# Optimization experiments

Measured on AMD Instinct MI355X. Metric: run time of the kernel, lower is better.

Reference implementation:

```python
import jax, jax.numpy as jnp
import numpy as np

LN_EPS = 1e-5  # torch LayerNorm default
MODES = 4


def setup_inputs() -> dict:
    key = jax.random.key(0)
    ks = jax.random.split(key, 5)
    B, S, H = 4, 4096, 1024
    nh, dk = 16, H // 16
    scale = 1.0 / (H * H)
    # frequency mode selection: random shuffle of range(S//2), take 4, sorted (seeded for determinism)
    rng = np.random.default_rng(0)
    index = jnp.asarray(np.sort(rng.permutation(S // 2)[:MODES]).astype(np.int32))
    return {
        "x": jax.random.normal(ks[0], (B, S, H), dtype=jnp.float32),
        "Wq": jax.random.normal(ks[1], (H, H), dtype=jnp.float32) * np.sqrt(2.0 / (H + dk)),
        "bq": jnp.zeros((H,), dtype=jnp.float32),
        "wr": scale * jax.random.uniform(ks[2], (nh, dk, dk, MODES), dtype=jnp.float32),
        "wi": scale * jax.random.uniform(ks[3], (nh, dk, dk, MODES), dtype=jnp.float32),
        "gamma": jnp.ones((H,), dtype=jnp.float32),
        "beta": jnp.zeros((H,), dtype=jnp.float32),
        "index": index,
    }


def reference(x, Wq, bq, wr, wi, gamma, beta, index):
    B, S, H = x.shape
    nh, dk = wr.shape[0], wr.shape[1]
    # q projection and head split: (B,S,H) -> (B,S,nh,dk) -> (B,nh,dk,S)
    q = (x @ Wq.T + bq).reshape(B, S, nh, dk).transpose(0, 2, 3, 1)
    x_ft = jnp.fft.rfft(q, axis=-1)                 # (B,nh,dk,S//2+1) complex
    xm = x_ft[..., index]                           # gather selected modes: (B,nh,dk,M)
    w = wr + 1j * wi                                # (nh,dk,dk,M) complex
    ym = jnp.einsum('bhim,hiom->bhom', xm, w)       # per-mode complex matmul
    # faithful: results written at slots 0..M-1 of out_ft (loop writes out_ft[...,wi])
    out_ft = jnp.zeros((B, nh, dk, S // 2 + 1), dtype=ym.dtype).at[..., :ym.shape[-1]].set(ym)
    x_if = jnp.fft.irfft(out_ft, n=S, axis=-1)      # (B,nh,dk,S) real
    # faithful permute(0,3,2,1).view: flattens as dk-major over heads
    out = x_if.transpose(0, 3, 2, 1).reshape(B, S, H)
    # dropout is identity in eval mode
    y = out + x
    mu = jnp.mean(y, axis=-1, keepdims=True)
    var = jnp.var(y, axis=-1, keepdims=True)
    return (y - mu) * jax.lax.rsqrt(var + LN_EPS) * gamma + beta
```

## Files before the change

### kernel.cpp

```cpp
#include <hip/hip_runtime.h>
#include <math.h>

#define BB 4
#define SS 4096
#define HH 1024
#define NH 16
#define DK 64
#define NMODES 4
#define NSB 128
#define SCHUNK (SS/NSB)
#define PPLANE ((size_t)BB * NSB * HH)
#define TWO_PI 6.28318530717958647692f

__global__ __launch_bounds__(256) void kA_dft(const float* __restrict__ x,
                                              const int* __restrict__ index,
                                              float* __restrict__ P) {
    __shared__ float tab[SCHUNK * 8];
    int t  = threadIdx.x;
    int sb = blockIdx.x & (NSB - 1);
    int b  = blockIdx.x >> 7;

    if (t < SCHUNK * NMODES) {
        int sl = t >> 2, m = t & 3;
        int k  = index[m];
        int sv = sb * SCHUNK + sl;
        int r  = (k * sv) & (SS - 1);
        float ang = (float)r * (TWO_PI / (float)SS);
        float sn, cs;
        sincosf(ang, &sn, &cs);
        tab[sl * 8 + m * 2]     = cs;
        tab[sl * 8 + m * 2 + 1] = sn;
    }
    __syncthreads();

    int c0 = t * 4;
    float acc[4][8];
    #pragma unroll
    for (int e = 0; e < 4; ++e)
        #pragma unroll
        for (int q = 0; q < 8; ++q) acc[e][q] = 0.f;

    const float* xp = x + ((size_t)(b * SS + sb * SCHUNK)) * HH + c0;
    #pragma unroll 8
    for (int r = 0; r < SCHUNK; ++r) {
        float4 xv = *(const float4*)(xp + (size_t)r * HH);
        float4 t0 = *(const float4*)&tab[r * 8];
        float4 t1 = *(const float4*)&tab[r * 8 + 4];
        float xe;
        #pragma unroll
        for (int e = 0; e < 4; ++e) {
            xe = (e == 0) ? xv.x : (e == 1) ? xv.y : (e == 2) ? xv.z : xv.w;
            acc[e][0] += xe * t0.x;  acc[e][1] -= xe * t0.y;
            acc[e][2] += xe * t0.z;  acc[e][3] -= xe * t0.w;
            acc[e][4] += xe * t1.x;  acc[e][5] -= xe * t1.y;
            acc[e][6] += xe * t1.z;  acc[e][7] -= xe * t1.w;
        }
    }
    size_t base = (size_t)(b * NSB + sb) * HH + c0;
    #pragma unroll
    for (int q = 0; q < 8; ++q) {
        *(float4*)&P[q * PPLANE + base] =
            make_float4(acc[0][q], acc[1][q], acc[2][q], acc[3][q]);
    }
}

__global__ __launch_bounds__(256) void kA2_reduce(const float* __restrict__ P,
                                                  float* __restrict__ G) {
    int i = blockIdx.x * 256 + threadIdx.x;
    int g = i >> 2;
    int quarter = i & 3;
    int j = g & (HH - 1);
    int q = (g >> 10) & 7;
    int b = g >> 13;
    const float* pp = P + q * PPLANE + (size_t)b * NSB * HH
                    + (size_t)(quarter * (NSB / 4)) * HH + j;
    float s = 0.f;
    #pragma unroll 16
    for (int sb = 0; sb < NSB / 4; ++sb)
        s += pp[(size_t)sb * HH];
    s += __shfl_xor(s, 1);
    s += __shfl_xor(s, 2);
    if (quarter == 0) G[g] = s;
}

__global__ __launch_bounds__(256) void kB_proj(const float* __restrict__ Wq,
                                               const float* __restrict__ bq,
                                               const int* __restrict__ index,
                                               const float* __restrict__ G,
                                               float* __restrict__ XM) {
    __shared__ float Gs[8 * HH];
    int t  = threadIdx.x;
    int cb = blockIdx.x & 63;
    int b  = blockIdx.x >> 6;
    {
        const float4* gsrc = (const float4*)(G + (size_t)b * 8 * HH);
        float4* gdst = (float4*)Gs;
        for (int u = t; u < 2 * HH; u += 256) gdst[u] = gsrc[u];
    }
    __syncthreads();

    int cl = t >> 4, jq = t & 15;
    int c = cb * 16 + cl;
    float acc[8] = {0.f,0.f,0.f,0.f,0.f,0.f,0.f,0.f};
    for (int j0 = jq * 4; j0 < HH; j0 += 64) {
        float4 wv = *(const float4*)&Wq[(size_t)c * HH + j0];
        #pragma unroll
        for (int q = 0; q < 8; ++q) {
            float4 gv = *(const float4*)&Gs[q * HH + j0];
            acc[q] += wv.x * gv.x + wv.y * gv.y + wv.z * gv.z + wv.w * gv.w;
        }
    }
    #pragma unroll
    for (int q = 0; q < 8; ++q) {
        acc[q] += __shfl_xor(acc[q], 1);
        acc[q] += __shfl_xor(acc[q], 2);
        acc[q] += __shfl_xor(acc[q], 4);
        acc[q] += __shfl_xor(acc[q], 8);
    }
    if (jq == 0) {
        float bias = bq[c];
        #pragma unroll
        for (int m = 0; m < NMODES; ++m)
            if (index[m] == 0) acc[2 * m] += bias * (float)SS;
        float* o = XM + ((size_t)(b * HH + c)) * 8;
        *(float4*)o       = make_float4(acc[0], acc[1], acc[2], acc[3]);
        *(float4*)(o + 4) = make_float4(acc[4], acc[5], acc[6], acc[7]);
    }
}

#define KC_IQ 8
#define KC_II (DK / KC_IQ)
__global__ __launch_bounds__(512) void kC_modes(const float* __restrict__ wr,
                                                const float* __restrict__ wi,
                                                const float* __restrict__ XM,
                                                float* __restrict__ CF) {
    __shared__ float xs[DK * 8];
    __shared__ float red[KC_IQ][DK][9];
    int t = threadIdx.x;
    int o = t & 63, iq = t >> 6;
    int h = blockIdx.x & 15;
    int b = blockIdx.x >> 4;
    for (int u = t; u < DK * 8; u += 512)
        xs[u] = XM[((size_t)(b * HH + h * DK)) * 8 + u];
    __syncthreads();

    float re[4] = {0.f,0.f,0.f,0.f}, im[4] = {0.f,0.f,0.f,0.f};
    #pragma unroll
    for (int ii = 0; ii < KC_II; ++ii) {
        int i = iq * KC_II + ii;
        float4 wrv = *(const float4*)&wr[(((size_t)(h * DK + i)) * DK + o) * 4];
        float4 wiv = *(const float4*)&wi[(((size_t)(h * DK + i)) * DK + o) * 4];
        float xr, xi;
        xr = xs[i * 8 + 0]; xi = xs[i * 8 + 1];
        re[0] += xr * wrv.x - xi * wiv.x;  im[0] += xr * wiv.x + xi * wrv.x;
        xr = xs[i * 8 + 2]; xi = xs[i * 8 + 3];
        re[1] += xr * wrv.y - xi * wiv.y;  im[1] += xr * wiv.y + xi * wrv.y;
        xr = xs[i * 8 + 4]; xi = xs[i * 8 + 5];
        re[2] += xr * wrv.z - xi * wiv.z;  im[2] += xr * wiv.z + xi * wrv.z;
        xr = xs[i * 8 + 6]; xi = xs[i * 8 + 7];
        re[3] += xr * wrv.w - xi * wiv.w;  im[3] += xr * wiv.w + xi * wrv.w;
    }
    #pragma unroll
    for (int m = 0; m < 4; ++m) {
        red[iq][o][2 * m]     = re[m];
        red[iq][o][2 * m + 1] = im[m];
    }
    __syncthreads();
    if (iq == 0) {
        float rr[8];
        #pragma unroll
        for (int q = 0; q < 8; ++q) {
            float s = 0.f;
            #pragma unroll
            for (int g = 0; g < KC_IQ; ++g) s += red[g][o][q];
            rr[q] = s;
        }
        int co = o * NH + h;
        const float inv = 1.0f / (float)SS;
        float* cp = CF + ((size_t)(b * HH + co)) * 8;
        cp[0] =  rr[0] * inv;
        cp[1] =  2.0f * rr[2] * inv;
        cp[2] = -2.0f * rr[3] * inv;
        cp[3] =  2.0f * rr[4] * inv;
        cp[4] = -2.0f * rr[5] * inv;
        cp[5] =  2.0f * rr[6] * inv;
        cp[6] = -2.0f * rr[7] * inv;
        cp[7] =  0.0f;
    }
}

#define KD_ROWS 8
__global__ __launch_bounds__(256) void kD_out(const float* __restrict__ x,
                                              const float* __restrict__ CF,
                                              const float* __restrict__ gamma,
                                              const float* __restrict__ beta,
                                              float* __restrict__ out) {
    __shared__ float trig[KD_ROWS][2];
    __shared__ float red[4][KD_ROWS][2];
    int t  = threadIdx.x;
    int b  = blockIdx.x >> 9;
    int s0 = (blockIdx.x & 511) * KD_ROWS;
    int c0 = t * 4;

    if (t < KD_ROWS) {
        float ang = (float)(s0 + t) * (TWO_PI / (float)SS);
        float sn, cs;
        sincosf(ang, &sn, &cs);
        trig[t][0] = cs;
        trig[t][1] = sn;
    }

    const float* cp = CF + (size_t)b * HH * 8 + (size_t)c0 * 8;
    float4 cfa[8];
    #pragma unroll
    for (int e = 0; e < 4; ++e) {
        cfa[2 * e]     = *(const float4*)(cp + e * 8);
        cfa[2 * e + 1] = *(const float4*)(cp + e * 8 + 4);
    }
    float4 g4 = *(const float4*)&gamma[c0];
    float4 b4 = *(const float4*)&beta[c0];
    int w = t >> 6, lane = t & 63;
    __syncthreads();

    float4 yv[KD_ROWS];
    #pragma unroll
    for (int r = 0; r < KD_ROWS; ++r) {
        int s = s0 + r;
        yv[r] = *(const float4*)&x[((size_t)(b * SS + s)) * HH + c0];
    }
    float sm[KD_ROWS], sq[KD_ROWS];
    #pragma unroll
    for (int r = 0; r < KD_ROWS; ++r) {
        float c1 = trig[r][0], s1 = trig[r][1];
        float c2 = c1 * c1 - s1 * s1, s2 = 2.f * s1 * c1;
        float c3 = c2 * c1 - s2 * s1, s3 = s2 * c1 + c2 * s1;
        float ye[4];
        #pragma unroll
        for (int e = 0; e < 4; ++e) {
            float xe = (e == 0) ? yv[r].x : (e == 1) ? yv[r].y
                     : (e == 2) ? yv[r].z : yv[r].w;
            float4 A = cfa[2 * e], Bv = cfa[2 * e + 1];
            ye[e] = xe + A.x + A.y * c1 + A.z * s1 + A.w * c2
                       + Bv.x * s2 + Bv.y * c3 + Bv.z * s3;
        }
        yv[r] = make_float4(ye[0], ye[1], ye[2], ye[3]);
        sm[r] = ye[0] + ye[1] + ye[2] + ye[3];
        sq[r] = ye[0]*ye[0] + ye[1]*ye[1] + ye[2]*ye[2] + ye[3]*ye[3];
    }
    #pragma unroll
    for (int off = 1; off < 64; off <<= 1) {
        #pragma unroll
        for (int r = 0; r < KD_ROWS; ++r) {
            sm[r] += __shfl_xor(sm[r], off);
            sq[r] += __shfl_xor(sq[r], off);
        }
    }
    if (lane == 0) {
        #pragma unroll
        for (int r = 0; r < KD_ROWS; ++r) {
            red[w][r][0] = sm[r];
            red[w][r][1] = sq[r];
        }
    }
    __syncthreads();
    #pragma unroll
    for (int r = 0; r < KD_ROWS; ++r) {
        int s = s0 + r;
        float tot  = red[0][r][0] + red[1][r][0] + red[2][r][0] + red[3][r][0];
        float totq = red[0][r][1] + red[1][r][1] + red[2][r][1] + red[3][r][1];
        float mean = tot * (1.0f / (float)HH);
        float var  = totq * (1.0f / (float)HH) - mean * mean;
        float rs = rsqrtf(var + 1e-5f);
        float4 o4;
        o4.x = (yv[r].x - mean) * rs * g4.x + b4.x;
        o4.y = (yv[r].y - mean) * rs * g4.y + b4.y;
        o4.z = (yv[r].z - mean) * rs * g4.z + b4.z;
        o4.w = (yv[r].w - mean) * rs * g4.w + b4.w;
        *(float4*)&out[((size_t)(b * SS + s)) * HH + c0] = o4;
    }
}

extern "C" void kernel_launch(void* const* d_in, const int* in_sizes, int n_in,
                              void* d_out, int out_size, void* d_ws, size_t ws_size,
                              hipStream_t stream) {
    const float* x     = (const float*)d_in[0];
    const float* Wq    = (const float*)d_in[1];
    const float* bq    = (const float*)d_in[2];
    const float* wr    = (const float*)d_in[3];
    const float* wi    = (const float*)d_in[4];
    const float* gamma = (const float*)d_in[5];
    const float* beta  = (const float*)d_in[6];
    const int*   index = (const int*)d_in[7];
    float* out = (float*)d_out;
    float* ws  = (float*)d_ws;

    const size_t nP     = PPLANE * 8;
    const size_t nSmall = (size_t)BB * HH * 8;

    float *P, *G, *XM, *CF;
    if (ws_size >= (nP + 3 * nSmall) * sizeof(float)) {
        P  = ws;
        G  = P + nP;
        XM = G + nSmall;
        CF = XM + nSmall;
    } else {
        P  = out;
        G  = ws;
        XM = G + nSmall;
        CF = XM + nSmall;
    }

    hipLaunchKernelGGL(kA_dft,     dim3(BB * NSB), dim3(256), 0, stream, x, index, P);
    hipLaunchKernelGGL(kA2_reduce, dim3(BB * HH * 8 * 4 / 256), dim3(256), 0, stream, P, G);
    hipLaunchKernelGGL(kB_proj,    dim3(BB * 64), dim3(256), 0, stream, Wq, bq, index, G, XM);
    hipLaunchKernelGGL(kC_modes,   dim3(BB * NH), dim3(512), 0, stream, wr, wi, XM, CF);
    hipLaunchKernelGGL(kD_out,     dim3(BB * (SS / KD_ROWS)), dim3(256), 0, stream, x, CF, gamma, beta, out);
}
```

Measured before the change: 58.63 us.

## Fuse DFT partial reduction in-block, merge projection and mode kernels, shuffle trig

```diff
diff --git a/kernel.cpp b/kernel.cpp
--- a/kernel.cpp
+++ b/kernel.cpp
@@ -7,23 +7,24 @@
 #define NH 16
 #define DK 64
 #define NMODES 4
-#define NSB 128
-#define SCHUNK (SS/NSB)
-#define PPLANE ((size_t)BB * NSB * HH)
 #define TWO_PI 6.28318530717958647692f
 
-__global__ __launch_bounds__(256) void kA_dft(const float* __restrict__ x,
+__global__ __launch_bounds__(512) void kA_dft(const float* __restrict__ x,
                                               const int* __restrict__ index,
-                                              float* __restrict__ P) {
-    __shared__ float tab[SCHUNK * 8];
-    int t  = threadIdx.x;
-    int sb = blockIdx.x & (NSB - 1);
-    int b  = blockIdx.x >> 7;
-
-    if (t < SCHUNK * NMODES) {
-        int sl = t >> 2, m = t & 3;
-        int k  = index[m];
-        int sv = sb * SCHUNK + sl;
+                                              float* __restrict__ Gp) {
+    __shared__ float tab[1024 * 8];
+    __shared__ float red[8][16][33];
+    int t   = threadIdx.x;
+    int bid = blockIdx.x;
+    int cb  = bid & 15;
+    int sq  = (bid >> 4) & 3;
+    int b   = bid >> 6;
+
+    int k0 = index[0], k1 = index[1], k2 = index[2], k3 = index[3];
+    for (int u = t; u < 4096; u += 512) {
+        int sl = u >> 2, m = u & 3;
+        int k  = (m == 0) ? k0 : (m == 1) ? k1 : (m == 2) ? k2 : k3;
+        int sv = sq * 1024 + sl;
         int r  = (k * sv) & (SS - 1);
         float ang = (float)r * (TWO_PI / (float)SS);
         float sn, cs;
@@ -33,19 +34,21 @@
     }
     __syncthreads();
 
-    int c0 = t * 4;
+    int c4 = t & 15, srow = t >> 4;
+    int c0 = cb * 64 + c4 * 4;
     float acc[4][8];
     #pragma unroll
     for (int e = 0; e < 4; ++e)
         #pragma unroll
         for (int q = 0; q < 8; ++q) acc[e][q] = 0.f;
 
-    const float* xp = x + ((size_t)(b * SS + sb * SCHUNK)) * HH + c0;
+    const float* xp = x + ((size_t)(b * SS + sq * 1024 + srow)) * HH + c0;
     #pragma unroll 8
-    for (int r = 0; r < SCHUNK; ++r) {
-        float4 xv = *(const float4*)(xp + (size_t)r * HH);
-        float4 t0 = *(const float4*)&tab[r * 8];
-        float4 t1 = *(const float4*)&tab[r * 8 + 4];
+    for (int pass = 0; pass < 32; ++pass) {
+        float4 xv = *(const float4*)(xp + (size_t)pass * 32 * HH);
+        int sl = pass * 32 + srow;
+        float4 t0 = *(const float4*)&tab[sl * 8];
+        float4 t1 = *(const float4*)&tab[sl * 8 + 4];
         float xe;
         #pragma unroll
         for (int e = 0; e < 4; ++e) {
@@ -56,136 +59,136 @@
             acc[e][6] += xe * t1.z;  acc[e][7] -= xe * t1.w;
         }
     }
-    size_t base = (size_t)(b * NSB + sb) * HH + c0;
-    #pragma unroll
-    for (int q = 0; q < 8; ++q) {
-        *(float4*)&P[q * PPLANE + base] =
-            make_float4(acc[0][q], acc[1][q], acc[2][q], acc[3][q]);
+    #pragma unroll
+    for (int e = 0; e < 4; ++e)
+        #pragma unroll
+        for (int q = 0; q < 8; ++q) {
+            acc[e][q] += __shfl_xor(acc[e][q], 16);
+            acc[e][q] += __shfl_xor(acc[e][q], 32);
+        }
+    int w = t >> 6, lane = t & 63;
+    if (lane < 16) {
+        #pragma unroll
+        for (int e = 0; e < 4; ++e)
+            #pragma unroll
+            for (int q = 0; q < 8; ++q)
+                red[w][lane][e * 8 + q] = acc[e][q];
+    }
+    __syncthreads();
+    {
+        int q = t >> 6, oc = t & 63;
+        float s = 0.f;
+        #pragma unroll
+        for (int w2 = 0; w2 < 8; ++w2)
+            s += red[w2][oc >> 2][(oc & 3) * 8 + q];
+        Gp[((size_t)((b * 4 + sq) * 8 + q)) * HH + cb * 64 + oc] = s;
     }
 }
 
-__global__ __launch_bounds__(256) void kA2_reduce(const float* __restrict__ P,
-                                                  float* __restrict__ G) {
-    int i = blockIdx.x * 256 + threadIdx.x;
-    int g = i >> 2;
-    int quarter = i & 3;
-    int j = g & (HH - 1);
-    int q = (g >> 10) & 7;
-    int b = g >> 13;
-    const float* pp = P + q * PPLANE + (size_t)b * NSB * HH
-                    + (size_t)(quarter * (NSB / 4)) * HH + j;
-    float s = 0.f;
-    #pragma unroll 16
-    for (int sb = 0; sb < NSB / 4; ++sb)
-        s += pp[(size_t)sb * HH];
-    s += __shfl_xor(s, 1);
-    s += __shfl_xor(s, 2);
-    if (quarter == 0) G[g] = s;
-}
-
-__global__ __launch_bounds__(256) void kB_proj(const float* __restrict__ Wq,
-                                               const float* __restrict__ bq,
-                                               const int* __restrict__ index,
-                                               const float* __restrict__ G,
-                                               float* __restrict__ XM) {
+__global__ __launch_bounds__(512) void kBC(const float* __restrict__ Gp,
+                                           const float* __restrict__ Wq,
+                                           const float* __restrict__ bq,
+                                           const int* __restrict__ index,
+                                           const float* __restrict__ wr,
+                                           const float* __restrict__ wi,
+                                           float* __restrict__ CF) {
     __shared__ float Gs[8 * HH];
-    int t  = threadIdx.x;
-    int cb = blockIdx.x & 63;
-    int b  = blockIdx.x >> 6;
-    {
-        const float4* gsrc = (const float4*)(G + (size_t)b * 8 * HH);
-        float4* gdst = (float4*)Gs;
-        for (int u = t; u < 2 * HH; u += 256) gdst[u] = gsrc[u];
-    }
-    __syncthreads();
-
-    int cl = t >> 4, jq = t & 15;
-    int c = cb * 16 + cl;
-    float acc[8] = {0.f,0.f,0.f,0.f,0.f,0.f,0.f,0.f};
-    for (int j0 = jq * 4; j0 < HH; j0 += 64) {
-        float4 wv = *(const float4*)&Wq[(size_t)c * HH + j0];
-        #pragma unroll
-        for (int q = 0; q < 8; ++q) {
-            float4 gv = *(const float4*)&Gs[q * HH + j0];
-            acc[q] += wv.x * gv.x + wv.y * gv.y + wv.z * gv.z + wv.w * gv.w;
-        }
-    }
-    #pragma unroll
-    for (int q = 0; q < 8; ++q) {
-        acc[q] += __shfl_xor(acc[q], 1);
-        acc[q] += __shfl_xor(acc[q], 2);
-        acc[q] += __shfl_xor(acc[q], 4);
-        acc[q] += __shfl_xor(acc[q], 8);
-    }
-    if (jq == 0) {
-        float bias = bq[c];
-        #pragma unroll
-        for (int m = 0; m < NMODES; ++m)
-            if (index[m] == 0) acc[2 * m] += bias * (float)SS;
-        float* o = XM + ((size_t)(b * HH + c)) * 8;
-        *(float4*)o       = make_float4(acc[0], acc[1], acc[2], acc[3]);
-        *(float4*)(o + 4) = make_float4(acc[4], acc[5], acc[6], acc[7]);
-    }
-}
-
-#define KC_IQ 8
-#define KC_II (DK / KC_IQ)
-__global__ __launch_bounds__(512) void kC_modes(const float* __restrict__ wr,
-                                                const float* __restrict__ wi,
-                                                const float* __restrict__ XM,
-                                                float* __restrict__ CF) {
     __shared__ float xs[DK * 8];
-    __shared__ float red[KC_IQ][DK][9];
+    __shared__ float red[8][DK][9];
     int t = threadIdx.x;
-    int o = t & 63, iq = t >> 6;
     int h = blockIdx.x & 15;
     int b = blockIdx.x >> 4;
-    for (int u = t; u < DK * 8; u += 512)
-        xs[u] = XM[((size_t)(b * HH + h * DK)) * 8 + u];
-    __syncthreads();
-
-    float re[4] = {0.f,0.f,0.f,0.f}, im[4] = {0.f,0.f,0.f,0.f};
-    #pragma unroll
-    for (int ii = 0; ii < KC_II; ++ii) {
-        int i = iq * KC_II + ii;
-        float4 wrv = *(const float4*)&wr[(((size_t)(h * DK + i)) * DK + o) * 4];
-        float4 wiv = *(const float4*)&wi[(((size_t)(h * DK + i)) * DK + o) * 4];
-        float xr, xi;
-        xr = xs[i * 8 + 0]; xi = xs[i * 8 + 1];
-        re[0] += xr * wrv.x - xi * wiv.x;  im[0] += xr * wiv.x + xi * wrv.x;
-        xr = xs[i * 8 + 2]; xi = xs[i * 8 + 3];
-        re[1] += xr * wrv.y - xi * wiv.y;  im[1] += xr * wiv.y + xi * wrv.y;
-        xr = xs[i * 8 + 4]; xi = xs[i * 8 + 5];
-        re[2] += xr * wrv.z - xi * wiv.z;  im[2] += xr * wiv.z + xi * wrv.z;
-        xr = xs[i * 8 + 6]; xi = xs[i * 8 + 7];
-        re[3] += xr * wrv.w - xi * wiv.w;  im[3] += xr * wiv.w + xi * wrv.w;
-    }
-    #pragma unroll
-    for (int m = 0; m < 4; ++m) {
-        red[iq][o][2 * m]     = re[m];
-        red[iq][o][2 * m + 1] = im[m];
-    }
-    __syncthreads();
-    if (iq == 0) {
-        float rr[8];
+
+    {
+        const float4* g0 = (const float4*)(Gp + (size_t)(b * 4 + 0) * 8 * HH);
+        const float4* g1 = (const float4*)(Gp + (size_t)(b * 4 + 1) * 8 * HH);
+        const float4* g2 = (const float4*)(Gp + (size_t)(b * 4 + 2) * 8 * HH);
+        const float4* g3 = (const float4*)(Gp + (size_t)(b * 4 + 3) * 8 * HH);
+        float4* gd = (float4*)Gs;
+        for (int u = t; u < 2 * HH; u += 512) {
+            float4 a = g0[u], b2 = g1[u], c = g2[u], d = g3[u];
+            gd[u] = make_float4(a.x + b2.x + c.x + d.x,
+                                a.y + b2.y + c.y + d.y,
+                                a.z + b2.z + c.z + d.z,
+                                a.w + b2.w + c.w + d.w);
+        }
+    }
+    __syncthreads();
+
+    {
+        int cl = t >> 3, jq = t & 7;
+        int c = h * DK + cl;
+        float acc[8] = {0.f,0.f,0.f,0.f,0.f,0.f,0.f,0.f};
+        for (int j0 = jq * 4; j0 < HH; j0 += 32) {
+            float4 wv = *(const float4*)&Wq[(size_t)c * HH + j0];
+            #pragma unroll
+            for (int q = 0; q < 8; ++q) {
+                float4 gv = *(const float4*)&Gs[q * HH + j0];
+                acc[q] += wv.x * gv.x + wv.y * gv.y + wv.z * gv.z + wv.w * gv.w;
+            }
+        }
         #pragma unroll
         for (int q = 0; q < 8; ++q) {
-            float s = 0.f;
-            #pragma unroll
-            for (int g = 0; g < KC_IQ; ++g) s += red[g][o][q];
-            rr[q] = s;
-        }
-        int co = o * NH + h;
-        const float inv = 1.0f / (float)SS;
-        float* cp = CF + ((size_t)(b * HH + co)) * 8;
-        cp[0] =  rr[0] * inv;
-        cp[1] =  2.0f * rr[2] * inv;
-        cp[2] = -2.0f * rr[3] * inv;
-        cp[3] =  2.0f * rr[4] * inv;
-        cp[4] = -2.0f * rr[5] * inv;
-        cp[5] =  2.0f * rr[6] * inv;
-        cp[6] = -2.0f * rr[7] * inv;
-        cp[7] =  0.0f;
+            acc[q] += __shfl_xor(acc[q], 1);
+            acc[q] += __shfl_xor(acc[q], 2);
+            acc[q] += __shfl_xor(acc[q], 4);
+        }
+        if (jq == 0) {
+            float bias = bq[c];
+            #pragma unroll
+            for (int m = 0; m < NMODES; ++m)
+                if (index[m] == 0) acc[2 * m] += bias * (float)SS;
+            #pragma unroll
+            for (int q = 0; q < 8; ++q) xs[cl * 8 + q] = acc[q];
+        }
+    }
+    __syncthreads();
+
+    {
+        int o = t & 63, iq = t >> 6;
+        float re[4] = {0.f,0.f,0.f,0.f}, im[4] = {0.f,0.f,0.f,0.f};
+        #pragma unroll
+        for (int ii = 0; ii < 8; ++ii) {
+            int i = iq * 8 + ii;
+            float4 wrv = *(const float4*)&wr[(((size_t)(h * DK + i)) * DK + o) * 4];
+            float4 wiv = *(const float4*)&wi[(((size_t)(h * DK + i)) * DK + o) * 4];
+            float xr, xi;
+            xr = xs[i * 8 + 0]; xi = xs[i * 8 + 1];
+            re[0] += xr * wrv.x - xi * wiv.x;  im[0] += xr * wiv.x + xi * wrv.x;
+            xr = xs[i * 8 + 2]; xi = xs[i * 8 + 3];
+            re[1] += xr * wrv.y - xi * wiv.y;  im[1] += xr * wiv.y + xi * wrv.y;
+            xr = xs[i * 8 + 4]; xi = xs[i * 8 + 5];
+            re[2] += xr * wrv.z - xi * wiv.z;  im[2] += xr * wiv.z + xi * wrv.z;
+            xr = xs[i * 8 + 6]; xi = xs[i * 8 + 7];
+            re[3] += xr * wrv.w - xi * wiv.w;  im[3] += xr * wiv.w + xi * wrv.w;
+        }
+        #pragma unroll
+        for (int m = 0; m < 4; ++m) {
+            red[iq][o][2 * m]     = re[m];
+            red[iq][o][2 * m + 1] = im[m];
+        }
+        __syncthreads();
+        if (iq == 0) {
+            float rr[8];
+            #pragma unroll
+            for (int q = 0; q < 8; ++q) {
+                float s = 0.f;
+                #pragma unroll
+                for (int g = 0; g < 8; ++g) s += red[g][o][q];
+                rr[q] = s;
+            }
+            int co = o * NH + h;
+            const float inv = 1.0f / (float)SS;
+            float* cp = CF + ((size_t)(b * HH + co)) * 8;
+            cp[0] =  rr[0] * inv;
+            cp[1] =  2.0f * rr[2] * inv;
+            cp[2] = -2.0f * rr[3] * inv;
+            cp[3] =  2.0f * rr[4] * inv;
+            cp[4] = -2.0f * rr[5] * inv;
+            cp[5] =  2.0f * rr[6] * inv;
+            cp[6] = -2.0f * rr[7] * inv;
+            cp[7] =  0.0f;
+        }
     }
 }
 
@@ -195,19 +198,16 @@
                                               const float* __restrict__ gamma,
                                               const float* __restrict__ beta,
                                               float* __restrict__ out) {
-    __shared__ float trig[KD_ROWS][2];
     __shared__ float red[4][KD_ROWS][2];
     int t  = threadIdx.x;
     int b  = blockIdx.x >> 9;
     int s0 = (blockIdx.x & 511) * KD_ROWS;
     int c0 = t * 4;
 
-    if (t < KD_ROWS) {
-        float ang = (float)(s0 + t) * (TWO_PI / (float)SS);
-        float sn, cs;
-        sincosf(ang, &sn, &cs);
-        trig[t][0] = cs;
-        trig[t][1] = sn;
+    float myc, mys;
+    {
+        float ang = (float)(s0 + (t & 7)) * (TWO_PI / (float)SS);
+        sincosf(ang, &mys, &myc);
     }
 
     const float* cp = CF + (size_t)b * HH * 8 + (size_t)c0 * 8;
@@ -220,7 +220,6 @@
     float4 g4 = *(const float4*)&gamma[c0];
     float4 b4 = *(const float4*)&beta[c0];
     int w = t >> 6, lane = t & 63;
-    __syncthreads();
 
     float4 yv[KD_ROWS];
     #pragma unroll
@@ -231,7 +230,7 @@
     float sm[KD_ROWS], sq[KD_ROWS];
     #pragma unroll
     for (int r = 0; r < KD_ROWS; ++r) {
-        float c1 = trig[r][0], s1 = trig[r][1];
+        float c1 = __shfl(myc, r), s1 = __shfl(mys, r);
         float c2 = c1 * c1 - s1 * s1, s2 = 2.f * s1 * c1;
         float c3 = c2 * c1 - s2 * s1, s3 = s2 * c1 + c2 * s1;
         float ye[4];
@@ -294,25 +293,21 @@
     float* out = (float*)d_out;
     float* ws  = (float*)d_ws;
 
-    const size_t nP     = PPLANE * 8;
-    const size_t nSmall = (size_t)BB * HH * 8;
-
-    float *P, *G, *XM, *CF;
-    if (ws_size >= (nP + 3 * nSmall) * sizeof(float)) {
-        P  = ws;
-        G  = P + nP;
-        XM = G + nSmall;
-        CF = XM + nSmall;
+    const size_t nGp = (size_t)BB * 4 * 8 * HH;
+    const size_t nCF = (size_t)BB * HH * 8;
+
+    float *Gp, *CFb;
+    if (ws_size >= (nGp + nCF) * sizeof(float)) {
+        Gp  = ws;
+        CFb = ws + nGp;
     } else {
-        P  = out;
-        G  = ws;
-        XM = G + nSmall;
-        CF = XM + nSmall;
-    }
-
-    hipLaunchKernelGGL(kA_dft,     dim3(BB * NSB), dim3(256), 0, stream, x, index, P);
-    hipLaunchKernelGGL(kA2_reduce, dim3(BB * HH * 8 * 4 / 256), dim3(256), 0, stream, P, G);
-    hipLaunchKernelGGL(kB_proj,    dim3(BB * 64), dim3(256), 0, stream, Wq, bq, index, G, XM);
-    hipLaunchKernelGGL(kC_modes,   dim3(BB * NH), dim3(512), 0, stream, wr, wi, XM, CF);
-    hipLaunchKernelGGL(kD_out,     dim3(BB * (SS / KD_ROWS)), dim3(256), 0, stream, x, CF, gamma, beta, out);
+        Gp  = out;
+        CFb = ws;
+    }
+
+    hipLaunchKernelGGL(kA_dft, dim3(BB * 64), dim3(512), 0, stream, x, index, Gp);
+    hipLaunchKernelGGL(kBC,    dim3(BB * NH), dim3(512), 0, stream,
+                       Gp, Wq, bq, index, wr, wi, CFb);
+    hipLaunchKernelGGL(kD_out, dim3(BB * (SS / KD_ROWS)), dim3(256), 0, stream,
+                       x, CFb, gamma, beta, out);
 }
```

Result: slower. 60.54 us (+3.2%).
